# Kernel optimization log

Hardware: AMD Instinct MI355X
Metric: run time of the kernel (lower is better)

Reference implementation:

```python
import jax, jax.numpy as jnp
import numpy as np

WINDOW = 512
STEP = 256
N_FREQ = 256
EPS = 1e-8


def setup_inputs() -> dict:
    key = jax.random.key(0)
    k1, k2, k3 = jax.random.split(key, 3)
    audio = jax.random.normal(k1, (512, 32768), dtype=jnp.float32)
    basis_real = jax.random.normal(k2, (N_FREQ, WINDOW), dtype=jnp.float32)
    basis_imag = jax.random.normal(k3, (N_FREQ, WINDOW), dtype=jnp.float32)
    return {"audio": audio, "basis_real": basis_real, "basis_imag": basis_imag}


def reference(audio, basis_real, basis_imag):
    # --- framing (windowed_audio): strided unfold -> [B, n_frames, WINDOW] ---
    n_samples = audio.shape[-1]
    n_frames = (n_samples - WINDOW) // STEP + 1  # 127 for 32768 samples
    idx = jnp.arange(n_frames)[:, None] * STEP + jnp.arange(WINDOW)[None, :]
    windowed = audio[:, idx]  # [B, F, W]

    # --- per-frame L2 normalization ---
    norms = jnp.linalg.norm(windowed, axis=-1, keepdims=True)  # [B, F, 1]
    wn = windowed / (norms + EPS)

    # --- basis normalization by complex L2 norm over window dim ---
    bnorm = jnp.sqrt(jnp.sum(basis_real * basis_real + basis_imag * basis_imag,
                             axis=-1, keepdims=True))  # [K, 1]
    br = basis_real / (bnorm + EPS)
    bi = basis_imag / (bnorm + EPS)

    # --- projection: windowed @ basis.T, real and imag parts ---
    real = jnp.einsum('bfw,kw->bfk', wn, br)  # [B, F, K]
    imag = jnp.einsum('bfw,kw->bfk', wn, bi)  # [B, F, K]
    return norms, real, imag
```

## Files before the change

### kernel.cpp

```cpp
#include <hip/hip_runtime.h>

#define WINDOW   512
#define STEPSZ   256
#define NFRAMES  127
#define NSAMP    32768
#define NBATCH   512
#define NFREQ    256
#define BM       128
#define SAMP_TILE 33024
#define NPS      129

typedef __attribute__((ext_vector_type(8)))  short short8;
typedef __attribute__((ext_vector_type(16))) float f32x16;
typedef __attribute__((ext_vector_type(4)))  float f4;

#define SWZ(byt) ((byt) ^ ((((byt) >> 9) & 7) << 4))

static __device__ __forceinline__ short f2bf(float x) {
    union { float f; unsigned u; } v; v.f = x;
    unsigned r = (v.u + 0x7fffu + ((v.u >> 16) & 1u)) >> 16;
    return (short)r;
}

__global__ __launch_bounds__(256) void prep_kernel(const float* __restrict__ br,
                                                   const float* __restrict__ bi,
                                                   short* __restrict__ Bf) {
    const int lane = threadIdx.x & 63;
    const int wid  = threadIdx.x >> 6;
    const int n    = blockIdx.x * 4 + wid;
    const float* pr = br + (size_t)n * WINDOW + lane * 8;
    const float* pi = bi + (size_t)n * WINDOW + lane * 8;
    f4 r0 = *(const f4*)pr;
    f4 r1 = *(const f4*)(pr + 4);
    f4 i0 = *(const f4*)pi;
    f4 i1 = *(const f4*)(pi + 4);
    float ss = 0.f;
#pragma unroll
    for (int j = 0; j < 4; ++j)
        ss += r0[j]*r0[j] + r1[j]*r1[j] + i0[j]*i0[j] + i1[j]*i1[j];
#pragma unroll
    for (int d = 1; d < 64; d <<= 1) ss += __shfl_xor(ss, d, 64);
    const float inv = 1.0f / (sqrtf(ss) + 1e-8f);
    short8 hr, hi;
#pragma unroll
    for (int j = 0; j < 4; ++j) {
        hr[j]     = f2bf(r0[j] * inv);
        hr[j + 4] = f2bf(r1[j] * inv);
        hi[j]     = f2bf(i0[j] * inv);
        hi[j + 4] = f2bf(i1[j] * inv);
    }
    const int ks  = lane >> 1, kg2 = lane & 1;
    const int nsR = n >> 5;
    const int nsI = 8 + (n >> 5);
    const int sl  = (n & 31) + 32 * kg2;
    *(short8*)(Bf + ((size_t)(nsR * 32 + ks) * 64 + sl) * 8) = hr;
    *(short8*)(Bf + ((size_t)(nsI * 32 + ks) * 64 + sl) * 8) = hi;
}

__global__ __launch_bounds__(1024, 4) void mel_kernel(const float* __restrict__ audio,
                                                      const short* __restrict__ Bf,
                                                      float* __restrict__ out) {
    __shared__ short smp[SAMP_TILE];
    __shared__ float ps[NPS];
    __shared__ float invn[BM];

    const int tid  = threadIdx.x;
    const int lane = tid & 63;
    const int wid  = tid >> 6;

    const int b = blockIdx.x;

    float* out_norms = out;
    float* out_real  = out + 65024;
    float* out_imag  = out + 65024 + 16646144;

    const float* abase = audio + (size_t)b * NSAMP;
    const int smax = NSAMP - 8;

    const int rl32 = lane & 31;
    const int kg2  = lane >> 5;
    const int wm   = wid >> 3;
    const int wn   = wid & 7;

    const short* bp0 = Bf + ((size_t)(2 * wn + 0) * 32 * 64 + lane) * 8;
    const short* bp1 = Bf + ((size_t)(2 * wn + 1) * 32 * 64 + lane) * 8;

    short8 bb[3][2];
#pragma unroll
    for (int d = 0; d < 3; ++d) {
        bb[d][0] = *(const short8*)(bp0 + (size_t)d * 512);
        bb[d][1] = *(const short8*)(bp1 + (size_t)d * 512);
    }

#pragma unroll
    for (int it = 0; it < 5; ++it) {
        const int sl = it * 8192 + tid * 8;
        float ss = 0.f;
        if (sl < SAMP_TILE) {
            const int slc = sl < smax ? sl : smax;
            f4 v0 = *(const f4*)(abase + slc);
            f4 v1 = *(const f4*)(abase + slc + 4);
            short8 h;
#pragma unroll
            for (int q = 0; q < 4; ++q) {
                ss += v0[q]*v0[q] + v1[q]*v1[q];
                h[q]     = f2bf(v0[q]);
                h[q + 4] = f2bf(v1[q]);
            }
            const int byt = sl * 2;
            *(short8*)((char*)smp + SWZ(byt)) = h;
        }
        ss += __shfl_xor(ss, 1, 64);
        ss += __shfl_xor(ss, 2, 64);
        ss += __shfl_xor(ss, 4, 64);
        ss += __shfl_xor(ss, 8, 64);
        ss += __shfl_xor(ss, 16, 64);
        const int chunk = (it * 8192 + tid * 8) >> 8;
        if ((tid & 31) == 0 && chunk < NPS) ps[chunk] = ss;
    }
    __syncthreads();

    if (tid < BM) {
        const float nrm = sqrtf(ps[tid] + ps[tid + 1]);
        if (tid < NFRAMES) out_norms[b * NFRAMES + tid] = nrm;
        invn[tid] = 1.0f / (nrm + 1e-8f);
    }

    const int rb0 = ((2 * wm + 0) * 32 + rl32) * 512 + kg2 * 16;
    const int rb1 = ((2 * wm + 1) * 32 + rl32) * 512 + kg2 * 16;
    const int X0  = (rl32 & 7) << 4;
    const int X1  = ((rl32 + 1) & 7) << 4;
    const char* sb = (const char*)smp;

    f32x16 acc[2][2];
    acc[0][0] = (f32x16)0.f; acc[0][1] = (f32x16)0.f;
    acc[1][0] = (f32x16)0.f; acc[1][1] = (f32x16)0.f;

#pragma unroll
    for (int ks = 0; ks < 32; ++ks) {
        const int X  = (ks < 16) ? X0 : X1;
        const int kb = ks * 32;
        short8 a0 = *(const short8*)(sb + ((rb0 + kb) ^ X));
        short8 a1 = *(const short8*)(sb + ((rb1 + kb) ^ X));
        const int cur = ks % 3;
        short8 cb0 = bb[cur][0];
        short8 cb1 = bb[cur][1];
        if (ks < 29) {
            bb[cur][0] = *(const short8*)(bp0 + (size_t)(ks + 3) * 512);
            bb[cur][1] = *(const short8*)(bp1 + (size_t)(ks + 3) * 512);
        }
        acc[0][0] = __builtin_amdgcn_mfma_f32_32x32x16_bf16(a0, cb0, acc[0][0], 0, 0, 0);
        acc[1][0] = __builtin_amdgcn_mfma_f32_32x32x16_bf16(a1, cb0, acc[1][0], 0, 0, 0);
        acc[0][1] = __builtin_amdgcn_mfma_f32_32x32x16_bf16(a0, cb1, acc[0][1], 0, 0, 0);
        acc[1][1] = __builtin_amdgcn_mfma_f32_32x32x16_bf16(a1, cb1, acc[1][1], 0, 0, 0);
    }
    __syncthreads();

#pragma unroll
    for (int mi = 0; mi < 2; ++mi) {
#pragma unroll
        for (int s = 0; s < 2; ++s) {
            const int n = (2 * wn + s) * 32 + rl32;
            float* dst = (n < NFREQ) ? out_real : out_imag;
            const int kcol = n & (NFREQ - 1);
            const int rbase = (2 * wm + mi) * 32 + 4 * kg2;
#pragma unroll
            for (int r = 0; r < 16; ++r) {
                const int fr = rbase + (r & 3) + 8 * (r >> 2);
                if (fr < NFRAMES)
                    dst[((size_t)b * NFRAMES + fr) * NFREQ + kcol] = acc[mi][s][r] * invn[fr];
            }
        }
    }
}

extern "C" void kernel_launch(void* const* d_in, const int* in_sizes, int n_in,
                              void* d_out, int out_size, void* d_ws, size_t ws_size,
                              hipStream_t stream) {
    const float* audio = (const float*)d_in[0];
    const float* br    = (const float*)d_in[1];
    const float* bi    = (const float*)d_in[2];
    float* out = (float*)d_out;
    short* Bf  = (short*)d_ws;

    prep_kernel<<<64, 256, 0, stream>>>(br, bi, Bf);
    mel_kernel<<<NBATCH, 1024, 0, stream>>>(audio, Bf, out);
}
```

Measured before the change: 64.24 us.

## Split into norms kernel and LDS-free GEMM reading audio directly from global

The fused per-batch kernel, which staged the whole audio row as bf16 in shared memory, is replaced by two kernels. A separate norms kernel writes per-frame inverse norms to workspace. The GEMM kernel then runs four smaller blocks per batch, loads A straight from global fp32, converts it to bf16 in registers with double-buffered prefetch, and uses a remapped block order. This removes the large LDS footprint and barriers so occupancy can rise, at the cost of an extra launch, re-reading audio twice (overlapping frames), and global loads on the MFMA critical path.

```diff
diff --git a/kernel.cpp b/kernel.cpp
--- a/kernel.cpp
+++ b/kernel.cpp
@@ -6,20 +6,22 @@
 #define NSAMP    32768
 #define NBATCH   512
 #define NFREQ    256
-#define BM       128
-#define SAMP_TILE 33024
-#define NPS      129
 
 typedef __attribute__((ext_vector_type(8)))  short short8;
 typedef __attribute__((ext_vector_type(16))) float f32x16;
 typedef __attribute__((ext_vector_type(4)))  float f4;
 
-#define SWZ(byt) ((byt) ^ ((((byt) >> 9) & 7) << 4))
-
 static __device__ __forceinline__ short f2bf(float x) {
     union { float f; unsigned u; } v; v.f = x;
     unsigned r = (v.u + 0x7fffu + ((v.u >> 16) & 1u)) >> 16;
     return (short)r;
+}
+
+static __device__ __forceinline__ short8 cvt8(f4 a, f4 b) {
+    short8 h;
+#pragma unroll
+    for (int q = 0; q < 4; ++q) { h[q] = f2bf(a[q]); h[q + 4] = f2bf(b[q]); }
+    return h;
 }
 
 __global__ __launch_bounds__(256) void prep_kernel(const float* __restrict__ br,
@@ -57,80 +59,82 @@
     *(short8*)(Bf + ((size_t)(nsI * 32 + ks) * 64 + sl) * 8) = hi;
 }
 
-__global__ __launch_bounds__(1024, 4) void mel_kernel(const float* __restrict__ audio,
-                                                      const short* __restrict__ Bf,
-                                                      float* __restrict__ out) {
-    __shared__ short smp[SAMP_TILE];
-    __shared__ float ps[NPS];
-    __shared__ float invn[BM];
-
-    const int tid  = threadIdx.x;
-    const int lane = tid & 63;
-    const int wid  = tid >> 6;
-
-    const int b = blockIdx.x;
-
-    float* out_norms = out;
-    float* out_real  = out + 65024;
-    float* out_imag  = out + 65024 + 16646144;
-
-    const float* abase = audio + (size_t)b * NSAMP;
-    const int smax = NSAMP - 8;
-
-    const int rl32 = lane & 31;
-    const int kg2  = lane >> 5;
-    const int wm   = wid >> 3;
-    const int wn   = wid & 7;
-
-    const short* bp0 = Bf + ((size_t)(2 * wn + 0) * 32 * 64 + lane) * 8;
-    const short* bp1 = Bf + ((size_t)(2 * wn + 1) * 32 * 64 + lane) * 8;
-
-    short8 bb[3][2];
+__global__ __launch_bounds__(512) void norms_kernel(const float* __restrict__ audio,
+                                                    float* __restrict__ invn_g,
+                                                    float* __restrict__ out_norms) {
+    __shared__ float ps[128];
+    const int tid = threadIdx.x;
+    const int b   = blockIdx.x;
+    const float* src = audio + (size_t)b * NSAMP;
 #pragma unroll
-    for (int d = 0; d < 3; ++d) {
-        bb[d][0] = *(const short8*)(bp0 + (size_t)d * 512);
-        bb[d][1] = *(const short8*)(bp1 + (size_t)d * 512);
-    }
-
+    for (int it = 0; it < 8; ++it) {
+        const int s = it * 4096 + tid * 8;
+        f4 v0 = *(const f4*)(src + s);
+        f4 v1 = *(const f4*)(src + s + 4);
+        float ss = 0.f;
 #pragma unroll
-    for (int it = 0; it < 5; ++it) {
-        const int sl = it * 8192 + tid * 8;
-        float ss = 0.f;
-        if (sl < SAMP_TILE) {
-            const int slc = sl < smax ? sl : smax;
-            f4 v0 = *(const f4*)(abase + slc);
-            f4 v1 = *(const f4*)(abase + slc + 4);
-            short8 h;
-#pragma unroll
-            for (int q = 0; q < 4; ++q) {
-                ss += v0[q]*v0[q] + v1[q]*v1[q];
-                h[q]     = f2bf(v0[q]);
-                h[q + 4] = f2bf(v1[q]);
-            }
-            const int byt = sl * 2;
-            *(short8*)((char*)smp + SWZ(byt)) = h;
-        }
+        for (int q = 0; q < 4; ++q) ss += v0[q]*v0[q] + v1[q]*v1[q];
         ss += __shfl_xor(ss, 1, 64);
         ss += __shfl_xor(ss, 2, 64);
         ss += __shfl_xor(ss, 4, 64);
         ss += __shfl_xor(ss, 8, 64);
         ss += __shfl_xor(ss, 16, 64);
-        const int chunk = (it * 8192 + tid * 8) >> 8;
-        if ((tid & 31) == 0 && chunk < NPS) ps[chunk] = ss;
+        if ((tid & 31) == 0) ps[s >> 8] = ss;
     }
     __syncthreads();
+    if (tid < NFRAMES) {
+        const float nrm = sqrtf(ps[tid] + ps[tid + 1]);
+        out_norms[b * NFRAMES + tid] = nrm;
+        invn_g[b * 128 + tid] = 1.0f / (nrm + 1e-8f);
+    } else if (tid == 127) {
+        invn_g[b * 128 + 127] = 0.0f;
+    }
+}
 
-    if (tid < BM) {
-        const float nrm = sqrtf(ps[tid] + ps[tid + 1]);
-        if (tid < NFRAMES) out_norms[b * NFRAMES + tid] = nrm;
-        invn[tid] = 1.0f / (nrm + 1e-8f);
-    }
+#define LDA(dA0, dA1, dB0, dB1, ks)                       \
+    dA0 = *(const f4*)(ap0 + (ks) * 16);                  \
+    dA1 = *(const f4*)(ap0 + (ks) * 16 + 4);              \
+    dB0 = *(const f4*)(ap1 + (ks) * 16);                  \
+    dB1 = *(const f4*)(ap1 + (ks) * 16 + 4);
+#define LDB(d0, d1, ks)                                   \
+    d0 = *(const short8*)(bp0 + (size_t)(ks) * 512);      \
+    d1 = *(const short8*)(bp1 + (size_t)(ks) * 512);
 
-    const int rb0 = ((2 * wm + 0) * 32 + rl32) * 512 + kg2 * 16;
-    const int rb1 = ((2 * wm + 1) * 32 + rl32) * 512 + kg2 * 16;
-    const int X0  = (rl32 & 7) << 4;
-    const int X1  = ((rl32 + 1) & 7) << 4;
-    const char* sb = (const char*)smp;
+__global__ __launch_bounds__(256, 3) void gemm_kernel(const float* __restrict__ audio,
+                                                      const short* __restrict__ Bf,
+                                                      const float* __restrict__ invn_g,
+                                                      float* __restrict__ out) {
+    const int tid  = threadIdx.x;
+    const int lane = tid & 63;
+    const int wid  = tid >> 6;
+
+    const int lb = (blockIdx.x & 7) * 256 + (blockIdx.x >> 3);
+    const int b  = lb >> 2;
+    const int q  = lb & 3;
+    const int mg = q & 1;
+    const int ng = (q >> 1) * 4 + wid;
+
+    const int rl32 = lane & 31;
+    const int kg2  = lane >> 5;
+
+    float* out_real = out + 65024;
+    float* out_imag = out + 65024 + 16646144;
+
+    const int r0 = mg * 64 + rl32;
+    int r1 = mg * 64 + 32 + rl32;
+    if (r1 > 126) r1 = 126;
+    const float* ap0 = audio + (size_t)b * NSAMP + r0 * 256 + kg2 * 8;
+    const float* ap1 = audio + (size_t)b * NSAMP + r1 * 256 + kg2 * 8;
+
+    const short* bp0 = Bf + ((size_t)(2 * ng + 0) * 32 * 64 + lane) * 8;
+    const short* bp1 = Bf + ((size_t)(2 * ng + 1) * 32 * 64 + lane) * 8;
+
+    f4 e0A, e0B, e1A, e1B, o0A, o0B, o1A, o1B;
+    short8 bE0, bE1, bO0, bO1;
+    LDA(e0A, e0B, e1A, e1B, 0)
+    LDB(bE0, bE1, 0)
+    LDA(o0A, o0B, o1A, o1B, 1)
+    LDB(bO0, bO1, 1)
 
     f32x16 acc[2][2];
     acc[0][0] = (f32x16)0.f; acc[0][1] = (f32x16)0.f;
@@ -138,37 +142,39 @@
 
 #pragma unroll
     for (int ks = 0; ks < 32; ++ks) {
-        const int X  = (ks < 16) ? X0 : X1;
-        const int kb = ks * 32;
-        short8 a0 = *(const short8*)(sb + ((rb0 + kb) ^ X));
-        short8 a1 = *(const short8*)(sb + ((rb1 + kb) ^ X));
-        const int cur = ks % 3;
-        short8 cb0 = bb[cur][0];
-        short8 cb1 = bb[cur][1];
-        if (ks < 29) {
-            bb[cur][0] = *(const short8*)(bp0 + (size_t)(ks + 3) * 512);
-            bb[cur][1] = *(const short8*)(bp1 + (size_t)(ks + 3) * 512);
+        short8 a0, a1, c0, c1;
+        if ((ks & 1) == 0) {
+            a0 = cvt8(e0A, e0B); a1 = cvt8(e1A, e1B);
+            c0 = bE0; c1 = bE1;
+            if (ks < 30) { LDA(e0A, e0B, e1A, e1B, ks + 2) LDB(bE0, bE1, ks + 2) }
+        } else {
+            a0 = cvt8(o0A, o0B); a1 = cvt8(o1A, o1B);
+            c0 = bO0; c1 = bO1;
+            if (ks < 30) { LDA(o0A, o0B, o1A, o1B, ks + 2) LDB(bO0, bO1, ks + 2) }
         }
-        acc[0][0] = __builtin_amdgcn_mfma_f32_32x32x16_bf16(a0, cb0, acc[0][0], 0, 0, 0);
-        acc[1][0] = __builtin_amdgcn_mfma_f32_32x32x16_bf16(a1, cb0, acc[1][0], 0, 0, 0);
-        acc[0][1] = __builtin_amdgcn_mfma_f32_32x32x16_bf16(a0, cb1, acc[0][1], 0, 0, 0);
-        acc[1][1] = __builtin_amdgcn_mfma_f32_32x32x16_bf16(a1, cb1, acc[1][1], 0, 0, 0);
+        acc[0][0] = __builtin_amdgcn_mfma_f32_32x32x16_bf16(a0, c0, acc[0][0], 0, 0, 0);
+        acc[1][0] = __builtin_amdgcn_mfma_f32_32x32x16_bf16(a1, c0, acc[1][0], 0, 0, 0);
+        acc[0][1] = __builtin_amdgcn_mfma_f32_32x32x16_bf16(a0, c1, acc[0][1], 0, 0, 0);
+        acc[1][1] = __builtin_amdgcn_mfma_f32_32x32x16_bf16(a1, c1, acc[1][1], 0, 0, 0);
     }
-    __syncthreads();
 
 #pragma unroll
     for (int mi = 0; mi < 2; ++mi) {
+        const int rbase = mg * 64 + mi * 32 + 4 * kg2;
+        float iv[16];
+#pragma unroll
+        for (int r = 0; r < 16; ++r)
+            iv[r] = invn_g[b * 128 + rbase + (r & 3) + 8 * (r >> 2)];
 #pragma unroll
         for (int s = 0; s < 2; ++s) {
-            const int n = (2 * wn + s) * 32 + rl32;
+            const int n = (2 * ng + s) * 32 + rl32;
             float* dst = (n < NFREQ) ? out_real : out_imag;
             const int kcol = n & (NFREQ - 1);
-            const int rbase = (2 * wm + mi) * 32 + 4 * kg2;
 #pragma unroll
             for (int r = 0; r < 16; ++r) {
                 const int fr = rbase + (r & 3) + 8 * (r >> 2);
                 if (fr < NFRAMES)
-                    dst[((size_t)b * NFRAMES + fr) * NFREQ + kcol] = acc[mi][s][r] * invn[fr];
+                    dst[((size_t)b * NFRAMES + fr) * NFREQ + kcol] = acc[mi][s][r] * iv[r];
             }
         }
     }
@@ -181,8 +187,10 @@
     const float* br    = (const float*)d_in[1];
     const float* bi    = (const float*)d_in[2];
     float* out = (float*)d_out;
-    short* Bf  = (short*)d_ws;
+    short* Bf     = (short*)d_ws;
+    float* invn_g = (float*)((char*)d_ws + (1 << 20));
 
     prep_kernel<<<64, 256, 0, stream>>>(br, bi, Bf);
-    mel_kernel<<<NBATCH, 1024, 0, stream>>>(audio, Bf, out);
+    norms_kernel<<<NBATCH, 512, 0, stream>>>(audio, invn_g, out);
+    gemm_kernel<<<NBATCH * 4, 256, 0, stream>>>(audio, Bf, invn_g, out);
 }
```

Measured after the change: 157.9 us. 2.46x slower.
